# Optimization experiments

Measured on AMD Instinct MI355X. Metric: run time of the kernel, lower is better.

Reference implementation:

```python
import jax, jax.numpy as jnp
import numpy as np

EPS = 1e-6


def setup_inputs() -> dict:
    key = jax.random.key(0)
    kx, kp = jax.random.split(key)
    B, D, P = 16384, 1024, 1024
    x = jax.random.normal(kx, (B, D), dtype=jnp.float32)
    prototypes = jax.random.normal(kp, (P, D), dtype=jnp.float32)
    return {"x": x, "prototypes": prototypes}


def reference(x, prototypes):
    # Vectorized form of the per-(sample, prototype) yat similarity:
    #   score[i, j] = <x_i, p_j>^2 / (||x_i - p_j||^2 + eps)
    # x: [B, D], prototypes: [P, D] -> scores: [B, P]
    x_flat = x.reshape(x.shape[0], -1)
    dots = jnp.einsum("bd,pd->bp", x_flat, prototypes)          # [B, P] GEMM
    x_sq = jnp.sum(x_flat * x_flat, axis=-1, keepdims=True)      # [B, 1]
    p_sq = jnp.sum(prototypes * prototypes, axis=-1)[None, :]    # [1, P]
    dist_sq = x_sq + p_sq - 2.0 * dots                            # ||x - p||^2
    scores = (dots * dots) / (dist_sq + EPS)
    return scores.astype(jnp.float32)
```

## Files before the change

### kernel.cpp

```cpp
#include <hip/hip_runtime.h>
#include <hip/hip_bf16.h>

#define EPS 1e-6f

typedef __attribute__((ext_vector_type(8))) __bf16 bf16x8;
typedef __attribute__((ext_vector_type(4))) float f32x4;

__device__ inline unsigned short f2bf_rtne(float f) {
    unsigned int u = __float_as_uint(f);
    unsigned int r = (u + 0x7FFFu + ((u >> 16) & 1u)) >> 16;
    return (unsigned short)r;
}

__global__ void split_all(const float* __restrict__ x, const float* __restrict__ p,
                          unsigned short* __restrict__ xhi, unsigned short* __restrict__ phi,
                          float* __restrict__ xsq, float* __restrict__ psq,
                          int B, int P, int D) {
    int wid = (blockIdx.x * blockDim.x + threadIdx.x) >> 6;
    int lane = threadIdx.x & 63;
    if (wid >= B + P) return;
    const float* in;
    unsigned short* hi;
    float* sq;
    if (wid < B) {
        in = x + (size_t)wid * D;
        hi = xhi + (size_t)wid * D;
        sq = xsq + wid;
    } else {
        int r = wid - B;
        in = p + (size_t)r * D;
        hi = phi + (size_t)r * D;
        sq = psq + r;
    }
    const float4* rp = (const float4*)in;
    ushort4* hp = (ushort4*)hi;
    float s = 0.f;
    int nvec = D >> 2;
    for (int j = lane; j < nvec; j += 64) {
        float4 v = rp[j];
        float fv[4] = {v.x, v.y, v.z, v.w};
        ushort4 h4;
        unsigned short* hh = (unsigned short*)&h4;
#pragma unroll
        for (int i = 0; i < 4; ++i) {
            float f = fv[i];
            s += f * f;
            hh[i] = f2bf_rtne(f);
        }
        hp[j] = h4;
    }
#pragma unroll
    for (int off = 32; off; off >>= 1) s += __shfl_down(s, off);
    if (lane == 0) *sq = s;
}

__global__ __launch_bounds__(512, 2) void yat_mfma8(
    const unsigned short* __restrict__ Ahi, const unsigned short* __restrict__ Phi,
    const float* __restrict__ xsq, const float* __restrict__ psq,
    float* __restrict__ out, int M, int N, int K) {

    __shared__ __align__(128) char sm[131072];
    const char* smc = (const char*)sm;

    const int t = threadIdx.x;
    const int lane = t & 63;
    const int wid = t >> 6;
    const int wm = wid >> 2;
    const int wn = wid & 3;

    const int nbx = N >> 8;
    const int nby = M >> 8;
    const int total = nbx * nby;
    int bid = blockIdx.x;
    bid = (bid & 7) * (total >> 3) + (bid >> 3);
    const int by = bid / nbx;
    const int bx = bid - by * nbx;
    const int brow = by << 8;
    const int bcol = bx << 8;

    const int NKT = K >> 6;
    const int NIT = NKT >> 1;

    f32x4 acc[8][4];
#pragma unroll
    for (int i = 0; i < 8; ++i)
#pragma unroll
        for (int j = 0; j < 4; ++j) acc[i][j] = (f32x4){0.f, 0.f, 0.f, 0.f};

    const int arow = lane & 15;
    const int kq16 = (lane >> 4) * 16;

    const int stg_colb = (((lane & 7) ^ (lane >> 3)) << 4);
    const size_t rowBytes = (size_t)K * 2;
    auto stage_ht = [&](int kt, int ht) {
        const int slot = kt & 1;
        const unsigned short* base;
        int rowbase;
        if (ht < 2) { base = Ahi; rowbase = brow; }
        else        { base = Phi; rowbase = bcol; }
        const size_t k0b = (size_t)kt << 7;
        const int half = ht & 1;
        char* lbase = (char*)sm + slot * 65536 + ((ht < 2) ? 0 : 32768) + half * 16384;
#pragma unroll
        for (int l = 0; l < 2; ++l) {
            int rl = (l * 8 + wid) * 8 + (lane >> 3);
            int grow = rowbase + half * 128 + rl;
            const char* src = (const char*)base + (size_t)grow * rowBytes + k0b + stg_colb;
            __builtin_amdgcn_global_load_lds(
                (const __attribute__((address_space(1))) void*)src,
                (__attribute__((address_space(3))) void*)(lbase + (l * 8 + wid) * 1024),
                16, 0, 0);
        }
    };

    bf16x8 af[4][2];
    bf16x8 bf0[2][2], bf1[2][2];

#define READ_A(slot, mh) do {                                                  \
    _Pragma("unroll")                                                          \
    for (int mi_ = 0; mi_ < 4; ++mi_) {                                        \
        int r_ = wm * 128 + (mh) * 64 + mi_ * 16 + arow;                       \
        const char* p_ = smc + (slot) * 65536 + r_ * 128;                      \
        int s_ = (r_ & 7) << 4;                                                \
        af[mi_][0] = *(const bf16x8*)(p_ + (kq16 ^ s_));                       \
        af[mi_][1] = *(const bf16x8*)(p_ + ((64 + kq16) ^ s_));                \
    }                                                                          \
} while (0)

#define READ_B(slot, nh, dst) do {                                             \
    _Pragma("unroll")                                                          \
    for (int ni_ = 0; ni_ < 2; ++ni_) {                                        \
        int r_ = wn * 64 + (nh) * 32 + ni_ * 16 + arow;                        \
        const char* p_ = smc + (slot) * 65536 + 32768 + r_ * 128;              \
        int s_ = (r_ & 7) << 4;                                                \
        dst[ni_][0] = *(const bf16x8*)(p_ + (kq16 ^ s_));                      \
        dst[ni_][1] = *(const bf16x8*)(p_ + ((64 + kq16) ^ s_));               \
    }                                                                          \
} while (0)

#define MFMA_Q(mh, nh, bset) do {                                              \
    __builtin_amdgcn_s_setprio(1);                                             \
    _Pragma("unroll")                                                          \
    for (int kk_ = 0; kk_ < 2; ++kk_)                                          \
        _Pragma("unroll")                                                      \
        for (int mi_ = 0; mi_ < 4; ++mi_)                                      \
            _Pragma("unroll")                                                  \
            for (int ni_ = 0; ni_ < 2; ++ni_)                                  \
                acc[(mh) * 4 + mi_][(nh) * 2 + ni_] =                          \
                    __builtin_amdgcn_mfma_f32_16x16x32_bf16(                   \
                        af[mi_][kk_], bset[ni_][kk_],                          \
                        acc[(mh) * 4 + mi_][(nh) * 2 + ni_], 0, 0, 0);         \
    __builtin_amdgcn_s_setprio(0);                                             \
} while (0)

#define PBAR() do {                                                            \
    __builtin_amdgcn_s_barrier();                                              \
    __builtin_amdgcn_sched_barrier(0);                                         \
    asm volatile("" ::: "memory");                                             \
} while (0)
#define VMCNT(n) asm volatile("s_waitcnt vmcnt(" #n ")" ::: "memory")

    stage_ht(0, 0); stage_ht(0, 1); stage_ht(0, 2); stage_ht(0, 3);
    stage_ht(1, 2); stage_ht(1, 3);
    VMCNT(4);
    PBAR();

    for (int it = 0; it < NIT; ++it) {
        const int T1 = 2 * it + 1, T2 = 2 * it + 2, T3 = 2 * it + 3;
        const bool more = (T2 < NKT);

        stage_ht(T1, 0);
        READ_A(0, 0); READ_B(0, 0, bf0);
        MFMA_Q(0, 0, bf0); PBAR();
        stage_ht(T1, 1);
        READ_B(0, 1, bf1);
        MFMA_Q(0, 1, bf1); PBAR();
        if (more) stage_ht(T2, 2);
        READ_A(0, 1);
        MFMA_Q(1, 0, bf0); PBAR();
        if (more) stage_ht(T2, 3);
        MFMA_Q(1, 1, bf1);
        if (more) { VMCNT(4); } else { VMCNT(0); }
        PBAR();

        if (more) stage_ht(T2, 0);
        READ_A(1, 0); READ_B(1, 0, bf0);
        MFMA_Q(0, 0, bf0); PBAR();
        if (more) stage_ht(T2, 1);
        READ_B(1, 1, bf1);
        MFMA_Q(0, 1, bf1); PBAR();
        if (more) stage_ht(T3, 2);
        READ_A(1, 1);
        MFMA_Q(1, 0, bf0); PBAR();
        if (more) stage_ht(T3, 3);
        MFMA_Q(1, 1, bf1);
        if (more) { VMCNT(4); }
        PBAR();
    }

#undef READ_A
#undef READ_B
#undef MFMA_Q
#undef PBAR
#undef VMCNT

    float* smf = (float*)sm;
#pragma unroll
    for (int pass = 0; pass < 2; ++pass) {
        __syncthreads();
        if (wm == pass) {
#pragma unroll
            for (int ni = 0; ni < 4; ++ni) {
                int lc = wn * 64 + ni * 16 + arow;
                float ps = psq[bcol + lc];
#pragma unroll
                for (int mi = 0; mi < 8; ++mi) {
                    f32x4 c = acc[mi][ni];
                    int lr0 = mi * 16 + (lane >> 4) * 4;
                    int grow0 = brow + pass * 128 + lr0;
                    float4 xs4 = *(const float4*)(xsq + grow0);
                    float xsv[4] = {xs4.x, xs4.y, xs4.z, xs4.w};
                    int lcs = lc ^ (((lr0 >> 2) & 1) << 4);
#pragma unroll
                    for (int j = 0; j < 4; ++j) {
                        float dv = c[j];
                        float denom = xsv[j] + ps - 2.0f * dv + EPS;
                        smf[(lr0 + j) * 256 + lcs] = dv * dv / denom;
                    }
                }
            }
        }
        __syncthreads();
#pragma unroll
        for (int rr = 0; rr < 16; ++rr) {
            int r = wid * 16 + rr;
            int swz = ((r >> 2) & 1) << 4;
            int c0 = lane * 4;
            f32x4 v = *(const f32x4*)(smf + r * 256 + (c0 ^ swz));
            *(f32x4*)(out + (size_t)(brow + pass * 128 + r) * N + bcol + c0) = v;
        }
    }
}

__global__ void yat_fallback(const float* __restrict__ x, const float* __restrict__ p,
                             float* __restrict__ out, int B, int P, int D) {
    __shared__ float xs[1024];
    int b = blockIdx.x;
    int pc = blockIdx.y * 256 + threadIdx.x;
    for (int i = threadIdx.x; i < D; i += 256) xs[i] = x[(size_t)b * D + i];
    __syncthreads();
    if (pc >= P) return;
    float dot = 0.f, psq = 0.f, xsq = 0.f;
    for (int k = 0; k < D; ++k) {
        float pv = p[(size_t)pc * D + k];
        float xv = xs[k];
        dot += xv * pv;
        psq += pv * pv;
        xsq += xv * xv;
    }
    float denom = xsq + psq - 2.f * dot + EPS;
    out[(size_t)b * P + pc] = dot * dot / denom;
}

extern "C" void kernel_launch(void* const* d_in, const int* in_sizes, int n_in,
                              void* d_out, int out_size, void* d_ws, size_t ws_size,
                              hipStream_t stream) {
    const float* x = (const float*)d_in[0];
    const float* p = (const float*)d_in[1];
    float* out = (float*)d_out;

    const int D = 1024;
    const int B = in_sizes[0] / D;
    const int P = in_sizes[1] / D;

    size_t need = ((size_t)B * D + (size_t)P * D) * 2 + ((size_t)B + P) * 4;
    int nblocks = (B / 256) * (P / 256);
    if (ws_size < need || (B % 256) || (P % 256) || (D % 64) || (nblocks % 8)) {
        yat_fallback<<<dim3(B, (P + 255) / 256), 256, 0, stream>>>(x, p, out, B, P, D);
        return;
    }

    unsigned short* xhi = (unsigned short*)d_ws;
    unsigned short* phi = xhi + (size_t)B * D;
    float* xsq = (float*)(phi + (size_t)P * D);
    float* psq = xsq + B;

    int nrows = B + P;
    split_all<<<(nrows + 3) / 4, 256, 0, stream>>>(x, p, xhi, phi, xsq, psq, B, P, D);

    yat_mfma8<<<dim3(nblocks), 512, 0, stream>>>(xhi, phi, xsq, psq, out, B, P, D);
}
```

Baseline: 72.02 us.

## Fuse bf16 conversion and norm computation into GEMM kernel, drop split pass

Removes the separate pre-pass that converted x and prototypes to bf16 and computed row norms. The GEMM kernel now loads fp32 tiles into registers, accumulates squared norms, converts to bf16 and writes to LDS with one-tile prefetch, using the norms from shared memory in the epilogue. This avoids a kernel launch and a round trip of bf16 copies through global memory. In exchange, each block reads fp32 data (double the bytes) redundantly across tiles, loses the async global-to-LDS loads, and raises register pressure.

```diff
diff --git a/kernel.cpp b/kernel.cpp
--- a/kernel.cpp
+++ b/kernel.cpp
@@ -6,60 +6,13 @@
 typedef __attribute__((ext_vector_type(8))) __bf16 bf16x8;
 typedef __attribute__((ext_vector_type(4))) float f32x4;
 
-__device__ inline unsigned short f2bf_rtne(float f) {
-    unsigned int u = __float_as_uint(f);
-    unsigned int r = (u + 0x7FFFu + ((u >> 16) & 1u)) >> 16;
-    return (unsigned short)r;
-}
-
-__global__ void split_all(const float* __restrict__ x, const float* __restrict__ p,
-                          unsigned short* __restrict__ xhi, unsigned short* __restrict__ phi,
-                          float* __restrict__ xsq, float* __restrict__ psq,
-                          int B, int P, int D) {
-    int wid = (blockIdx.x * blockDim.x + threadIdx.x) >> 6;
-    int lane = threadIdx.x & 63;
-    if (wid >= B + P) return;
-    const float* in;
-    unsigned short* hi;
-    float* sq;
-    if (wid < B) {
-        in = x + (size_t)wid * D;
-        hi = xhi + (size_t)wid * D;
-        sq = xsq + wid;
-    } else {
-        int r = wid - B;
-        in = p + (size_t)r * D;
-        hi = phi + (size_t)r * D;
-        sq = psq + r;
-    }
-    const float4* rp = (const float4*)in;
-    ushort4* hp = (ushort4*)hi;
-    float s = 0.f;
-    int nvec = D >> 2;
-    for (int j = lane; j < nvec; j += 64) {
-        float4 v = rp[j];
-        float fv[4] = {v.x, v.y, v.z, v.w};
-        ushort4 h4;
-        unsigned short* hh = (unsigned short*)&h4;
-#pragma unroll
-        for (int i = 0; i < 4; ++i) {
-            float f = fv[i];
-            s += f * f;
-            hh[i] = f2bf_rtne(f);
-        }
-        hp[j] = h4;
-    }
-#pragma unroll
-    for (int off = 32; off; off >>= 1) s += __shfl_down(s, off);
-    if (lane == 0) *sq = s;
-}
-
-__global__ __launch_bounds__(512, 2) void yat_mfma8(
-    const unsigned short* __restrict__ Ahi, const unsigned short* __restrict__ Phi,
-    const float* __restrict__ xsq, const float* __restrict__ psq,
+__global__ __launch_bounds__(512, 2) void yat_fused(
+    const float* __restrict__ X, const float* __restrict__ Pr,
     float* __restrict__ out, int M, int N, int K) {
 
     __shared__ __align__(128) char sm[131072];
+    __shared__ float sqx[256];
+    __shared__ float sqp[256];
     const char* smc = (const char*)sm;
 
     const int t = threadIdx.x;
@@ -79,7 +32,6 @@
     const int bcol = bx << 8;
 
     const int NKT = K >> 6;
-    const int NIT = NKT >> 1;
 
     f32x4 acc[8][4];
 #pragma unroll
@@ -90,31 +42,54 @@
     const int arow = lane & 15;
     const int kq16 = (lane >> 4) * 16;
 
-    const int stg_colb = (((lane & 7) ^ (lane >> 3)) << 4);
-    const size_t rowBytes = (size_t)K * 2;
-    auto stage_ht = [&](int kt, int ht) {
-        const int slot = kt & 1;
-        const unsigned short* base;
-        int rowbase;
-        if (ht < 2) { base = Ahi; rowbase = brow; }
-        else        { base = Phi; rowbase = bcol; }
-        const size_t k0b = (size_t)kt << 7;
-        const int half = ht & 1;
-        char* lbase = (char*)sm + slot * 65536 + ((ht < 2) ? 0 : 32768) + half * 16384;
+    const int rsub = lane >> 3;
+    const int lc = (lane & 7) ^ rsub;
+    int offA[2][2], offB[2][2];
+    int dofA[2][2], dofB[2][2];
+#pragma unroll
+    for (int hh = 0; hh < 2; ++hh)
 #pragma unroll
         for (int l = 0; l < 2; ++l) {
-            int rl = (l * 8 + wid) * 8 + (lane >> 3);
-            int grow = rowbase + half * 128 + rl;
-            const char* src = (const char*)base + (size_t)grow * rowBytes + k0b + stg_colb;
-            __builtin_amdgcn_global_load_lds(
-                (const __attribute__((address_space(1))) void*)src,
-                (__attribute__((address_space(3))) void*)(lbase + (l * 8 + wid) * 1024),
-                16, 0, 0);
-        }
-    };
-
-    bf16x8 af[4][2];
-    bf16x8 bf0[2][2], bf1[2][2];
+            int rl = (l * 8 + wid) * 8 + rsub;
+            offA[hh][l] = (brow + hh * 128 + rl) * K + lc * 8;
+            offB[hh][l] = (bcol + hh * 128 + rl) * K + lc * 8;
+            dofA[hh][l] = hh * 16384 + (l * 8 + wid) * 1024 + lane * 16;
+            dofB[hh][l] = 32768 + hh * 16384 + (l * 8 + wid) * 1024 + lane * 16;
+        }
+
+    f32x4 sA[2][2][2], sB[2][2][2];
+    float qA[2][2] = {{0.f, 0.f}, {0.f, 0.f}};
+    float qB[2][2] = {{0.f, 0.f}, {0.f, 0.f}};
+
+#define ISSUE(kt1) do {                                                        \
+    _Pragma("unroll")                                                          \
+    for (int hh_ = 0; hh_ < 2; ++hh_)                                          \
+        _Pragma("unroll")                                                      \
+        for (int l_ = 0; l_ < 2; ++l_) {                                       \
+            sA[hh_][l_][0] = *(const f32x4*)(X + offA[hh_][l_] + (kt1) * 64);  \
+            sA[hh_][l_][1] = *(const f32x4*)(X + offA[hh_][l_] + (kt1) * 64 + 4);\
+            sB[hh_][l_][0] = *(const f32x4*)(Pr + offB[hh_][l_] + (kt1) * 64); \
+            sB[hh_][l_][1] = *(const f32x4*)(Pr + offB[hh_][l_] + (kt1) * 64 + 4);\
+        }                                                                      \
+} while (0)
+
+#define CVTWRITE(slot, S, Q, DOF) do {                                         \
+    _Pragma("unroll")                                                          \
+    for (int hh_ = 0; hh_ < 2; ++hh_)                                          \
+        _Pragma("unroll")                                                      \
+        for (int l_ = 0; l_ < 2; ++l_) {                                       \
+            f32x4 u_ = S[hh_][l_][0], v_ = S[hh_][l_][1];                      \
+            Q[hh_][l_] += u_[0]*u_[0] + u_[1]*u_[1] + u_[2]*u_[2] + u_[3]*u_[3]\
+                        + v_[0]*v_[0] + v_[1]*v_[1] + v_[2]*v_[2] + v_[3]*v_[3];\
+            bf16x8 pk_;                                                        \
+            _Pragma("unroll")                                                  \
+            for (int i_ = 0; i_ < 4; ++i_) {                                   \
+                pk_[i_]     = (__bf16)u_[i_];                                  \
+                pk_[4 + i_] = (__bf16)v_[i_];                                  \
+            }                                                                  \
+            *(bf16x8*)((char*)sm + (slot) * 65536 + DOF[hh_][l_]) = pk_;       \
+        }                                                                      \
+} while (0)
 
 #define READ_A(slot, mh) do {                                                  \
     _Pragma("unroll")                                                          \
@@ -158,51 +133,59 @@
     __builtin_amdgcn_sched_barrier(0);                                         \
     asm volatile("" ::: "memory");                                             \
 } while (0)
-#define VMCNT(n) asm volatile("s_waitcnt vmcnt(" #n ")" ::: "memory")
-
-    stage_ht(0, 0); stage_ht(0, 1); stage_ht(0, 2); stage_ht(0, 3);
-    stage_ht(1, 2); stage_ht(1, 3);
-    VMCNT(4);
+#define LGKMDRAIN() asm volatile("s_waitcnt lgkmcnt(0)" ::: "memory")
+
+    bf16x8 af[4][2];
+    bf16x8 bf0[2][2], bf1[2][2];
+
+    ISSUE(0);
+    CVTWRITE(0, sA, qA, dofA);
+    CVTWRITE(0, sB, qB, dofB);
+    LGKMDRAIN();
     PBAR();
 
-    for (int it = 0; it < NIT; ++it) {
-        const int T1 = 2 * it + 1, T2 = 2 * it + 2, T3 = 2 * it + 3;
-        const bool more = (T2 < NKT);
-
-        stage_ht(T1, 0);
-        READ_A(0, 0); READ_B(0, 0, bf0);
+    for (int kt = 0; kt < NKT; ++kt) {
+        const int slot = kt & 1;
+        const bool more = (kt + 1) < NKT;
+
+        if (more) ISSUE(kt + 1);
+        READ_A(slot, 0); READ_B(slot, 0, bf0);
         MFMA_Q(0, 0, bf0); PBAR();
-        stage_ht(T1, 1);
-        READ_B(0, 1, bf1);
+        READ_B(slot, 1, bf1);
         MFMA_Q(0, 1, bf1); PBAR();
-        if (more) stage_ht(T2, 2);
-        READ_A(0, 1);
+        if (more) CVTWRITE(slot ^ 1, sA, qA, dofA);
+        READ_A(slot, 1);
         MFMA_Q(1, 0, bf0); PBAR();
-        if (more) stage_ht(T2, 3);
+        if (more) CVTWRITE(slot ^ 1, sB, qB, dofB);
         MFMA_Q(1, 1, bf1);
-        if (more) { VMCNT(4); } else { VMCNT(0); }
+        LGKMDRAIN();
         PBAR();
-
-        if (more) stage_ht(T2, 0);
-        READ_A(1, 0); READ_B(1, 0, bf0);
-        MFMA_Q(0, 0, bf0); PBAR();
-        if (more) stage_ht(T2, 1);
-        READ_B(1, 1, bf1);
-        MFMA_Q(0, 1, bf1); PBAR();
-        if (more) stage_ht(T3, 2);
-        READ_A(1, 1);
-        MFMA_Q(1, 0, bf0); PBAR();
-        if (more) stage_ht(T3, 3);
-        MFMA_Q(1, 1, bf1);
-        if (more) { VMCNT(4); }
-        PBAR();
-    }
-
+    }
+
+#undef ISSUE
+#undef CVTWRITE
 #undef READ_A
 #undef READ_B
 #undef MFMA_Q
 #undef PBAR
-#undef VMCNT
+#undef LGKMDRAIN
+
+#pragma unroll
+    for (int hh = 0; hh < 2; ++hh)
+#pragma unroll
+        for (int l = 0; l < 2; ++l) {
+            float a = qA[hh][l], b = qB[hh][l];
+#pragma unroll
+            for (int m = 1; m <= 4; m <<= 1) {
+                a += __shfl_xor(a, m);
+                b += __shfl_xor(b, m);
+            }
+            if ((lane & 7) == 0) {
+                int r = hh * 128 + l * 64 + wid * 8 + rsub;
+                sqx[r] = a;
+                sqp[r] = b;
+            }
+        }
 
     float* smf = (float*)sm;
 #pragma unroll
@@ -211,20 +194,18 @@
         if (wm == pass) {
 #pragma unroll
             for (int ni = 0; ni < 4; ++ni) {
-                int lc = wn * 64 + ni * 16 + arow;
-                float ps = psq[bcol + lc];
+                int lcc = wn * 64 + ni * 16 + arow;
+                float ps = sqp[lcc];
 #pragma unroll
                 for (int mi = 0; mi < 8; ++mi) {
                     f32x4 c = acc[mi][ni];
                     int lr0 = mi * 16 + (lane >> 4) * 4;
-                    int grow0 = brow + pass * 128 + lr0;
-                    float4 xs4 = *(const float4*)(xsq + grow0);
-                    float xsv[4] = {xs4.x, xs4.y, xs4.z, xs4.w};
-                    int lcs = lc ^ (((lr0 >> 2) & 1) << 4);
+                    f32x4 xs4 = *(const f32x4*)(&sqx[pass * 128 + lr0]);
+                    int lcs = lcc ^ (((lr0 >> 2) & 1) << 4);
 #pragma unroll
                     for (int j = 0; j < 4; ++j) {
                         float dv = c[j];
-                        float denom = xsv[j] + ps - 2.0f * dv + EPS;
+                        float denom = xs4[j] + ps - 2.0f * dv + EPS;
                         smf[(lr0 + j) * 256 + lcs] = dv * dv / denom;
                     }
                 }
@@ -273,20 +254,11 @@
     const int B = in_sizes[0] / D;
     const int P = in_sizes[1] / D;
 
-    size_t need = ((size_t)B * D + (size_t)P * D) * 2 + ((size_t)B + P) * 4;
     int nblocks = (B / 256) * (P / 256);
-    if (ws_size < need || (B % 256) || (P % 256) || (D % 64) || (nblocks % 8)) {
+    if ((B % 256) || (P % 256) || (D % 64) || (nblocks % 8)) {
         yat_fallback<<<dim3(B, (P + 255) / 256), 256, 0, stream>>>(x, p, out, B, P, D);
         return;
     }
 
-    unsigned short* xhi = (unsigned short*)d_ws;
-    unsigned short* phi = xhi + (size_t)B * D;
-    float* xsq = (float*)(phi + (size_t)P * D);
-    float* psq = xsq + B;
-
-    int nrows = B + P;
-    split_all<<<(nrows + 3) / 4, 256, 0, stream>>>(x, p, xhi, phi, xsq, psq, B, P, D);
-
-    yat_mfma8<<<dim3(nblocks), 512, 0, stream>>>(xhi, phi, xsq, psq, out, B, P, D);
+    yat_fused<<<dim3(nblocks), 512, 0, stream>>>(x, p, out, B, P, D);
 }
```

Result: slower. 157.0 us (+117.9%).
